# Optimization experiments

Measured on AMD Instinct MI355X. Metric: run time of the kernel, lower is better.

The kernel has to match this reference:

```python
import jax, jax.numpy as jnp
import numpy as np

H_WINDOW = 8
X_WINDOW = 8
H_LAG = 0
X_LAG = 0
CHANNELS = 1
B, T = 8192, 2048


def setup_inputs() -> dict:
    key = jax.random.key(0)
    k1, k2, k3 = jax.random.split(key, 3)
    h = jax.random.normal(k1, (B, T, 1), dtype=jnp.float32)
    # torch init: normal(0, 0.05)
    h_weights = 0.05 * jax.random.normal(k2, (H_WINDOW, CHANNELS), dtype=jnp.float32)
    x_weights = 0.05 * jax.random.normal(k3, (X_WINDOW, CHANNELS), dtype=jnp.float32)
    biases = jnp.zeros((1, CHANNELS), dtype=jnp.float32)
    return {"h": h, "h_weights": h_weights, "x_weights": x_weights, "biases": biases}


def reference(h, h_weights, x_weights, biases):
    b, t, _ = h.shape
    start_ix = max(H_WINDOW + H_LAG - 1, X_WINDOW, X_LAG - 1)
    h_t = jnp.transpose(h, (1, 0, 2))              # [T, B, 1] time-major for per-step gather
    hw0 = h[:, :H_WINDOW].reshape(b, H_WINDOW)     # initial h window
    xw0 = jnp.zeros((b, X_WINDOW), dtype=h.dtype)  # initial x window (zeros, as in torch)

    def step(carry, i):
        hw_, xw_ = carry  # [B, H_WINDOW], [B, X_WINDOW]
        out = xw_ @ x_weights + hw_ @ h_weights + biases  # [B, CHANNELS]
        # window updates; at the final step the torch code skips the update but the
        # carry is discarded, so an index-clamped unconditional update is equivalent
        idx = jnp.minimum(i + 1 - H_LAG, t - 1)
        hw_n = jnp.concatenate([hw_, h_t[idx]], axis=1)[:, -H_WINDOW:]
        xw_n = jnp.concatenate([xw_, out], axis=1)[:, -X_WINDOW:]
        return (hw_n, xw_n), out

    _, outs = jax.lax.scan(step, (hw0, xw0), jnp.arange(start_ix, t))  # [T-start_ix, B, C]
    output = jnp.zeros((b, t, CHANNELS), dtype=h.dtype)
    output = output.at[:, start_ix:].set(jnp.transpose(outs, (1, 0, 2)))
    return output
```

## Files before the change

kernel.cpp:

```cpp
#include <hip/hip_runtime.h>


typedef float  f32x4  __attribute__((ext_vector_type(4)));
typedef short  bf16x8 __attribute__((ext_vector_type(8)));

#define TT 2048
#define BB 8192
#define LK 64
#define NTAPS 71
#define LROW 584

__device__ __forceinline__ unsigned f2bfu(float x) {
    unsigned u = __float_as_uint(x);
    return (u + 0x7FFFu + ((u >> 16) & 1u)) >> 16;
}
__device__ __forceinline__ float bf2f(short s) {
    return __uint_as_float(((unsigned)(unsigned short)s) << 16);
}

__device__ __forceinline__ void group8(const float hwt[8], const float xwt[8],
                                       float bs, const float win[8],
                                       const float nh[8], const float xq[8],
                                       float res[8])
{
#pragma unroll
    for (int u = 0; u < 8; ++u) {
        float acc = bs;
#pragma unroll
        for (int k = u; k < 8; ++k) acc = fmaf(win[k], hwt[k - u], acc);
#pragma unroll
        for (int k = 0; k < u; ++k) acc = fmaf(nh[k], hwt[8 - u + k], acc);
#pragma unroll
        for (int k = u; k < 8; ++k) acc = fmaf(xq[k], xwt[k - u], acc);
#pragma unroll
        for (int k = 0; k < u; ++k) acc = fmaf(res[k], xwt[8 - u + k], acc);
        res[u] = acc;
    }
}

__global__ __launch_bounds__(256) void rr_fused(
    const float* __restrict__ h, const float* __restrict__ hwt_g,
    const float* __restrict__ xwt_g, const float* __restrict__ bias_g,
    float* __restrict__ out)
{
    __shared__ short hlds[16][LROW];
    __shared__ float cl[NTAPS + 1];

    const int t   = threadIdx.x;
    const int bid = blockIdx.x;
    const int s   = bid & 3;
    const int r0  = (bid >> 2) << 4;

    const int ts     = (s < 3) ? (5 + 31 * s) : 98;
    const int ntiles = (s < 3) ? 31 : 30;
    const int gcol0  = 16 * ts - 80;
    const int nf4    = (s < 3) ? 144 : 140;

    if (t < 192) {
        const int row = t / 12;
        const int l12 = t - row * 12;
        const float* hrow = h + (size_t)(r0 + row) * TT + gcol0;
#pragma unroll 4
        for (int k = 0; k < 12; ++k) {
            const int c = l12 + 12 * k;
            if (c < nf4) {
                float4 v = reinterpret_cast<const float4*>(hrow)[c];
                uint2 pk;
                asm("v_cvt_pk_bf16_f32 %0, %1, %2" : "=v"(pk.x) : "v"(v.x), "v"(v.y));
                asm("v_cvt_pk_bf16_f32 %0, %1, %2" : "=v"(pk.y) : "v"(v.z), "v"(v.w));
                *reinterpret_cast<uint2*>(&hlds[row][4 * c]) = pk;
            }
        }
    } else {
        const int l = t - 192;
        float xw[8], hw[8];
#pragma unroll
        for (int j = 0; j < 8; ++j) { xw[j] = xwt_g[j]; hw[j] = hwt_g[j]; }
        float w[8];
#pragma unroll
        for (int j = 0; j < 8; ++j) w[j] = 0.f;
        float c1 = 0.f, c2 = 0.f, ksum = 0.f;
        for (int n = 0; n <= NTAPS; ++n) {
            float dsel = 0.f;
#pragma unroll
            for (int j = 0; j < 8; ++j) dsel = fmaf(hw[j], w[j], dsel);
            if (n == l + 1)  c1 = dsel;
            if (n == l + 65) c2 = dsel;
            float k = 0.f;
#pragma unroll
            for (int j = 0; j < 8; ++j) k = fmaf(xw[j], w[j], k);
            if (n == 0) k = 1.f;
            ksum += k;
#pragma unroll
            for (int j = 0; j < 7; ++j) w[j] = w[j + 1];
            w[7] = k;
        }
        cl[l] = c1;
        if (l < 7) cl[64 + l] = c2;
        if (l == 7) cl[NTAPS] = bias_g[0] * ksum;
    }
    __syncthreads();

    const int lane = t & 63;
    const int v16  = lane & 15;
    const int gq   = lane >> 4;
    const int w    = t >> 6;

    const float biasK = cl[NTAPS];

    if (s == 0 && t < 16) {
        float* orow = out + (size_t)(r0 + t) * TT;
        float hwt[8], xwt[8];
#pragma unroll
        for (int j = 0; j < 8; ++j) { hwt[j] = hwt_g[j]; xwt[j] = xwt_g[j]; }
        const float bs = bias_g[0];
        float win[8], xq[8];
#pragma unroll
        for (int j = 0; j < 8; ++j) { win[j] = bf2f(hlds[t][j]); xq[j] = 0.f; }
        float4 z = make_float4(0.f, 0.f, 0.f, 0.f);
        reinterpret_cast<float4*>(orow)[0] = z;
        reinterpret_cast<float4*>(orow)[1] = z;
        for (int g = 8; g < 80; g += 8) {
            float nh[8], res[8];
#pragma unroll
            for (int j = 0; j < 8; ++j) nh[j] = bf2f(hlds[t][g + 1 + j]);
            group8(hwt, xwt, bs, win, nh, xq, res);
            float4* d4 = reinterpret_cast<float4*>(orow + g);
            d4[0] = make_float4(res[0], res[1], res[2], res[3]);
            d4[1] = make_float4(res[4], res[5], res[6], res[7]);
#pragma unroll
            for (int j = 0; j < 8; ++j) { win[j] = nh[j]; xq[j] = res[j]; }
        }
    }

    bf16x8 bfr[3];
#pragma unroll
    for (int kb = 0; kb < 3; ++kb) {
#pragma unroll
        for (int e = 0; e < 8; ++e) {
            const int idx = 80 + v16 - 32 * kb - 8 * gq - e;
            const float val = (idx >= 0 && idx < NTAPS) ? cl[idx] : 0.f;
            bfr[kb][e] = (short)f2bfu(val);
        }
    }

    for (int tl = w; tl < ntiles; tl += 4) {
        const int colb = 16 * tl;
        f32x4 acc = {biasK, biasK, biasK, biasK};
#pragma unroll
        for (int kb = 0; kb < 3; ++kb) {
            const bf16x8 a = *reinterpret_cast<const bf16x8*>(
                &hlds[v16][colb + 32 * kb + 8 * gq]);
            acc = __builtin_amdgcn_mfma_f32_16x16x32_bf16(bfr[kb], a, acc, 0, 0, 0);
        }
        const int i0 = (ts + tl) * 16;
        float* ob = out + (size_t)(r0 + v16) * TT + i0 + 4 * gq;
        *reinterpret_cast<f32x4*>(ob) = acc;
    }
}

extern "C" void kernel_launch(void* const* d_in, const int* in_sizes, int n_in,
                              void* d_out, int out_size, void* d_ws, size_t ws_size,
                              hipStream_t stream) {
    const float* h    = (const float*)d_in[0];
    const float* hwt  = (const float*)d_in[1];
    const float* xwt  = (const float*)d_in[2];
    const float* bias = (const float*)d_in[3];
    float* out = (float*)d_out;
    rr_fused<<<(BB / 16) * 4, 256, 0, stream>>>(h, hwt, xwt, bias, out);
}
```

Measured before the change: 29.08 us.

## Process multiple row groups per block with double-buffered LDS prefetch

Each block now handles four consecutive 16-row groups instead of one, so the tap-coefficient computation and B-fragment setup are amortized across more work. The next group's input is loaded into registers while the current group's sequential prefix and MFMA tiles run, then converted to bf16 into a second LDS buffer. This trades a quarter as many blocks (less parallelism, 512 blocks) and extra LDS and registers for lower per-block setup cost and overlapped loads.

```diff
diff --git a/kernel.cpp b/kernel.cpp
--- a/kernel.cpp
+++ b/kernel.cpp
@@ -9,6 +9,7 @@
 #define LK 64
 #define NTAPS 71
 #define LROW 584
+#define GCH 4
 
 __device__ __forceinline__ unsigned f2bfu(float x) {
     unsigned u = __float_as_uint(x);
@@ -38,18 +39,19 @@
     }
 }
 
-__global__ __launch_bounds__(256) void rr_fused(
+__global__ __launch_bounds__(256) void rr_persist(
     const float* __restrict__ h, const float* __restrict__ hwt_g,
     const float* __restrict__ xwt_g, const float* __restrict__ bias_g,
     float* __restrict__ out)
 {
-    __shared__ short hlds[16][LROW];
+    __shared__ short hlds[2][16][LROW];
     __shared__ float cl[NTAPS + 1];
 
-    const int t   = threadIdx.x;
-    const int bid = blockIdx.x;
-    const int s   = bid & 3;
-    const int r0  = (bid >> 2) << 4;
+    const int t     = threadIdx.x;
+    const int bid   = blockIdx.x;
+    const int s     = bid & 3;
+    const int chain = bid >> 2;
+    const int r0b   = chain * (16 * GCH);
 
     const int ts     = (s < 3) ? (5 + 31 * s) : 98;
     const int ntiles = (s < 3) ? 31 : 30;
@@ -59,7 +61,7 @@
     if (t < 192) {
         const int row = t / 12;
         const int l12 = t - row * 12;
-        const float* hrow = h + (size_t)(r0 + row) * TT + gcol0;
+        const float* hrow = h + (size_t)(r0b + row) * TT + gcol0;
 #pragma unroll 4
         for (int k = 0; k < 12; ++k) {
             const int c = l12 + 12 * k;
@@ -68,7 +70,7 @@
                 uint2 pk;
                 asm("v_cvt_pk_bf16_f32 %0, %1, %2" : "=v"(pk.x) : "v"(v.x), "v"(v.y));
                 asm("v_cvt_pk_bf16_f32 %0, %1, %2" : "=v"(pk.y) : "v"(v.z), "v"(v.w));
-                *reinterpret_cast<uint2*>(&hlds[row][4 * c]) = pk;
+                *reinterpret_cast<uint2*>(&hlds[0][row][4 * c]) = pk;
             }
         }
     } else {
@@ -108,31 +110,6 @@
 
     const float biasK = cl[NTAPS];
 
-    if (s == 0 && t < 16) {
-        float* orow = out + (size_t)(r0 + t) * TT;
-        float hwt[8], xwt[8];
-#pragma unroll
-        for (int j = 0; j < 8; ++j) { hwt[j] = hwt_g[j]; xwt[j] = xwt_g[j]; }
-        const float bs = bias_g[0];
-        float win[8], xq[8];
-#pragma unroll
-        for (int j = 0; j < 8; ++j) { win[j] = bf2f(hlds[t][j]); xq[j] = 0.f; }
-        float4 z = make_float4(0.f, 0.f, 0.f, 0.f);
-        reinterpret_cast<float4*>(orow)[0] = z;
-        reinterpret_cast<float4*>(orow)[1] = z;
-        for (int g = 8; g < 80; g += 8) {
-            float nh[8], res[8];
-#pragma unroll
-            for (int j = 0; j < 8; ++j) nh[j] = bf2f(hlds[t][g + 1 + j]);
-            group8(hwt, xwt, bs, win, nh, xq, res);
-            float4* d4 = reinterpret_cast<float4*>(orow + g);
-            d4[0] = make_float4(res[0], res[1], res[2], res[3]);
-            d4[1] = make_float4(res[4], res[5], res[6], res[7]);
-#pragma unroll
-            for (int j = 0; j < 8; ++j) { win[j] = nh[j]; xq[j] = res[j]; }
-        }
-    }
-
     bf16x8 bfr[3];
 #pragma unroll
     for (int kb = 0; kb < 3; ++kb) {
@@ -144,18 +121,76 @@
         }
     }
 
-    for (int tl = w; tl < ntiles; tl += 4) {
-        const int colb = 16 * tl;
-        f32x4 acc = {biasK, biasK, biasK, biasK};
-#pragma unroll
-        for (int kb = 0; kb < 3; ++kb) {
-            const bf16x8 a = *reinterpret_cast<const bf16x8*>(
-                &hlds[v16][colb + 32 * kb + 8 * gq]);
-            acc = __builtin_amdgcn_mfma_f32_16x16x32_bf16(bfr[kb], a, acc, 0, 0, 0);
-        }
-        const int i0 = (ts + tl) * 16;
-        float* ob = out + (size_t)(r0 + v16) * TT + i0 + 4 * gq;
-        *reinterpret_cast<f32x4*>(ob) = acc;
+    const int srow = t >> 4;
+    const int l16  = t & 15;
+
+    for (int g = 0; g < GCH; ++g) {
+        const int cur = g & 1;
+        const int r0  = r0b + 16 * g;
+
+        float4 pre[9];
+        if (g + 1 < GCH) {
+            const float* hrow = h + (size_t)(r0 + 16 + srow) * TT + gcol0;
+#pragma unroll
+            for (int k = 0; k < 9; ++k) {
+                const int c = l16 + 16 * k;
+                pre[k] = (c < nf4) ? reinterpret_cast<const float4*>(hrow)[c]
+                                   : make_float4(0.f, 0.f, 0.f, 0.f);
+            }
+        }
+
+        if (s == 0 && t < 16) {
+            float* orow = out + (size_t)(r0 + t) * TT;
+            float hwt[8], xwt[8];
+#pragma unroll
+            for (int j = 0; j < 8; ++j) { hwt[j] = hwt_g[j]; xwt[j] = xwt_g[j]; }
+            const float bs = bias_g[0];
+            float win[8], xq[8];
+#pragma unroll
+            for (int j = 0; j < 8; ++j) { win[j] = bf2f(hlds[cur][t][j]); xq[j] = 0.f; }
+            float4 z = make_float4(0.f, 0.f, 0.f, 0.f);
+            reinterpret_cast<float4*>(orow)[0] = z;
+            reinterpret_cast<float4*>(orow)[1] = z;
+            for (int gg = 8; gg < 80; gg += 8) {
+                float nh[8], res[8];
+#pragma unroll
+                for (int j = 0; j < 8; ++j) nh[j] = bf2f(hlds[cur][t][gg + 1 + j]);
+                group8(hwt, xwt, bs, win, nh, xq, res);
+                float4* d4 = reinterpret_cast<float4*>(orow + gg);
+                d4[0] = make_float4(res[0], res[1], res[2], res[3]);
+                d4[1] = make_float4(res[4], res[5], res[6], res[7]);
+#pragma unroll
+                for (int j = 0; j < 8; ++j) { win[j] = nh[j]; xq[j] = res[j]; }
+            }
+        }
+
+        for (int tl = w; tl < ntiles; tl += 4) {
+            const int colb = 16 * tl;
+            f32x4 acc = {biasK, biasK, biasK, biasK};
+#pragma unroll
+            for (int kb = 0; kb < 3; ++kb) {
+                const bf16x8 a = *reinterpret_cast<const bf16x8*>(
+                    &hlds[cur][v16][colb + 32 * kb + 8 * gq]);
+                acc = __builtin_amdgcn_mfma_f32_16x16x32_bf16(bfr[kb], a, acc, 0, 0, 0);
+            }
+            const int i0 = (ts + tl) * 16;
+            float* ob = out + (size_t)(r0 + v16) * TT + i0 + 4 * gq;
+            *reinterpret_cast<f32x4*>(ob) = acc;
+        }
+
+        if (g + 1 < GCH) {
+#pragma unroll
+            for (int k = 0; k < 9; ++k) {
+                const int c = l16 + 16 * k;
+                if (c < nf4) {
+                    uint2 pk;
+                    asm("v_cvt_pk_bf16_f32 %0, %1, %2" : "=v"(pk.x) : "v"(pre[k].x), "v"(pre[k].y));
+                    asm("v_cvt_pk_bf16_f32 %0, %1, %2" : "=v"(pk.y) : "v"(pre[k].z), "v"(pre[k].w));
+                    *reinterpret_cast<uint2*>(&hlds[cur ^ 1][srow][4 * c]) = pk;
+                }
+            }
+        }
+        __syncthreads();
     }
 }
 
@@ -167,5 +202,5 @@
     const float* xwt  = (const float*)d_in[2];
     const float* bias = (const float*)d_in[3];
     float* out = (float*)d_out;
-    rr_fused<<<(BB / 16) * 4, 256, 0, stream>>>(h, hwt, xwt, bias, out);
-}
+    rr_persist<<<(BB / (16 * GCH)) * 4, 256, 0, stream>>>(h, hwt, xwt, bias, out);
+}
```

Result: slower. 39.05 us (+34.3%).
